# Optimization experiments

Measured on AMD Instinct MI355X. Metric: run time of the kernel, lower is better.

Reference implementation:

```python
import jax, jax.numpy as jnp
import numpy as np

B, S, HID = 1, 4096, 2048
NH, NKV, HD, RD = 16, 4, 128, 64
EPS = 1e-6
SCALE = HD ** -0.5


def _rmsnorm(x, w, eps=EPS):
    x32 = x.astype(jnp.float32)
    var = jnp.mean(x32 * x32, axis=-1, keepdims=True)
    return (w * (x32 * jax.lax.rsqrt(var + eps))).astype(x.dtype)


def _rotate_half(x):
    x1, x2 = jnp.split(x, 2, axis=-1)
    return jnp.concatenate([-x2, x1], axis=-1)


def setup_inputs() -> dict:
    key = jax.random.key(0)
    ks = jax.random.split(key, 6)
    hidden_states = jax.random.normal(ks[0], (B, S, HID), dtype=jnp.float32)
    # real rotary embeddings for rotary_dim=RD
    inv_freq = 1.0 / (10000.0 ** (jnp.arange(0, RD, 2, dtype=jnp.float32) / RD))
    pos = jnp.arange(S, dtype=jnp.float32)
    freqs = pos[:, None] * inv_freq[None, :]          # [S, RD/2]
    emb = jnp.concatenate([freqs, freqs], axis=-1)     # [S, RD]
    cos = jnp.cos(emb)[None]                           # [1, S, RD]
    sin = jnp.sin(emb)[None]
    w = 0.02
    Wq = jax.random.normal(ks[1], (NH * HD, HID), dtype=jnp.float32) * w
    Wk = jax.random.normal(ks[2], (NKV * HD, HID), dtype=jnp.float32) * w
    Wv = jax.random.normal(ks[3], (NKV * HD, HID), dtype=jnp.float32) * w
    Wo = jax.random.normal(ks[4], (HID, NH * HD), dtype=jnp.float32) * w
    q_norm_w = jnp.ones((NH * HD,), dtype=jnp.float32)
    k_norm_w = jnp.ones((NKV * HD,), dtype=jnp.float32)
    return {"hidden_states": hidden_states, "cos": cos, "sin": sin,
            "Wq": Wq, "Wk": Wk, "Wv": Wv, "Wo": Wo,
            "q_norm_w": q_norm_w, "k_norm_w": k_norm_w}


def _attention(hidden_states, cos, sin, Wq, Wk, Wv, Wo, q_norm_w, k_norm_w):
    bsz, q_len, _ = hidden_states.shape
    q = hidden_states @ Wq.T                 # [B,S,NH*HD]
    k = hidden_states @ Wk.T                 # [B,S,NKV*HD]
    v = hidden_states @ Wv.T
    q = _rmsnorm(q, q_norm_w)
    k = _rmsnorm(k, k_norm_w)
    q = q.reshape(bsz, q_len, NH, HD).transpose(0, 2, 1, 3)   # b h s d
    k = k.reshape(bsz, q_len, NKV, HD).transpose(0, 2, 1, 3)
    v = v.reshape(bsz, q_len, NKV, HD).transpose(0, 2, 1, 3)
    # partial RoPE on first RD dims
    c = cos[:, None]  # [B,1,S,RD]
    s = sin[:, None]
    q_rot, q_pass = q[..., :RD], q[..., RD:]
    k_rot, k_pass = k[..., :RD], k[..., RD:]
    q = jnp.concatenate([q_rot * c + _rotate_half(q_rot) * s, q_pass], axis=-1)
    k = jnp.concatenate([k_rot * c + _rotate_half(k_rot) * s, k_pass], axis=-1)
    # GQA: repeat kv heads
    n_rep = NH // NKV
    k = jnp.repeat(k, n_rep, axis=1)
    v = jnp.repeat(v, n_rep, axis=1)
    scores = jnp.einsum('bhqd,bhkd->bhqk', q, k) * SCALE
    causal = jnp.triu(jnp.full((q_len, q_len), -jnp.inf, dtype=scores.dtype), k=1)
    scores = scores + causal
    probs = jax.nn.softmax(scores.astype(jnp.float32), axis=-1).astype(q.dtype)
    out = jnp.einsum('bhqk,bhkd->bhqd', probs, v)
    out = out.transpose(0, 2, 1, 3).reshape(bsz, q_len, NH * HD)
    return out @ Wo.T


def reference(hidden_states, cos, sin, Wq, Wk, Wv, Wo, q_norm_w, k_norm_w):
    return _attention(hidden_states, cos, sin, Wq, Wk, Wv, Wo, q_norm_w, k_norm_w)
```

## Files before the change

kernel.cpp:

```cpp
#include <hip/hip_runtime.h>

typedef unsigned short u16;
typedef unsigned int   u32;
typedef __bf16 bf16x8 __attribute__((ext_vector_type(8)));
typedef float  f32x4  __attribute__((ext_vector_type(4)));

#define S_LEN 4096
#define HIDN  2048
#define NHEAD 16
#define NKVH  4
#define HDIM  128
#define ROTD  64
#define QKVN  3072

__device__ __forceinline__ u16 f2bf(float f) {
  union { float f; u32 u; } v; v.f = f;
  u32 r = v.u + 0x7FFFu + ((v.u >> 16) & 1u);
  return (u16)(r >> 16);
}
__device__ __forceinline__ u16 f2bf_fast(float f) {
  union { __bf16 b; u16 u; } cv; cv.b = (__bf16)f; return cv.u;
}
__device__ __forceinline__ float bf2f(u16 u) {
  union { u32 u; float f; } v; v.u = ((u32)u) << 16; return v.f;
}
__device__ __forceinline__ void gl2lds16(const u16* g, u16* l) {
  __builtin_amdgcn_global_load_lds((const __attribute__((address_space(1))) void*)g,
                                   (__attribute__((address_space(3))) void*)l, 16, 0, 0);
}
__device__ __forceinline__ f32x4 mfma_bf16(bf16x8 a, bf16x8 b, f32x4 c) {
  return __builtin_amdgcn_mfma_f32_16x16x32_bf16(a, b, c, 0, 0, 0);
}
template <int N> __device__ __forceinline__ void vmwait() {
  if constexpr (N == 7)      asm volatile("s_waitcnt vmcnt(7)" ::: "memory");
  else if constexpr (N == 6) asm volatile("s_waitcnt vmcnt(6)" ::: "memory");
  else                       asm volatile("s_waitcnt vmcnt(0)" ::: "memory");
}

__global__ __launch_bounds__(256) void cvt4_f32_bf16(const float* __restrict__ h,
                                                     const float* __restrict__ Wq,
                                                     const float* __restrict__ Wk,
                                                     const float* __restrict__ Wv,
                                                     u16* __restrict__ hbf,
                                                     u16* __restrict__ wqkv) {
  const int b = blockIdx.x;
  const float* src; u16* dst;
  if (b < 4096)      { src = h  + (size_t)b * 2048;           dst = hbf  + (size_t)b * 2048; }
  else if (b < 6144) { src = Wq + (size_t)(b - 4096) * 2048;  dst = wqkv + (size_t)(b - 4096) * 2048; }
  else if (b < 6656) { src = Wk + (size_t)(b - 6144) * 2048;  dst = wqkv + 4194304u + (size_t)(b - 6144) * 2048; }
  else               { src = Wv + (size_t)(b - 6656) * 2048;  dst = wqkv + 5242880u + (size_t)(b - 6656) * 2048; }
  size_t i = (size_t)threadIdx.x * 8;
  float4 a = *(const float4*)(src + i);
  float4 c = *(const float4*)(src + i + 4);
  uint4 r;
  r.x = (u32)f2bf(a.x) | ((u32)f2bf(a.y) << 16);
  r.y = (u32)f2bf(a.z) | ((u32)f2bf(a.w) << 16);
  r.z = (u32)f2bf(c.x) | ((u32)f2bf(c.y) << 16);
  r.w = (u32)f2bf(c.z) | ((u32)f2bf(c.w) << 16);
  *(uint4*)(dst + i) = r;
}

__global__ __launch_bounds__(256) void cvt_f32_bf16(const float* __restrict__ in,
                                                    u16* __restrict__ out) {
  size_t i = ((size_t)blockIdx.x * 256 + threadIdx.x) * 8;
  float4 a = *(const float4*)(in + i);
  float4 b = *(const float4*)(in + i + 4);
  uint4 r;
  r.x = (u32)f2bf(a.x) | ((u32)f2bf(a.y) << 16);
  r.y = (u32)f2bf(a.z) | ((u32)f2bf(a.w) << 16);
  r.z = (u32)f2bf(b.x) | ((u32)f2bf(b.y) << 16);
  r.w = (u32)f2bf(b.z) | ((u32)f2bf(b.w) << 16);
  *(uint4*)(out + i) = r;
}

template <int BN, int NB, bool BF16OUT>
__global__ __launch_bounds__(512, 2) void gemm_big(const u16* __restrict__ A,
                                                   const u16* __restrict__ Bm,
                                                   void* __restrict__ Cp,
                                                   int M, int N, int K) {
  constexpr int WNC = BN / 4;
  constexpr int NF  = WNC / 16;
  constexpr int ASZ = 256 * 128;
  constexpr int BUF = ASZ + BN * 128;
  constexpr int LOADS = 4 + NB;
  __shared__ __align__(1024) char lds[2 * BUF];

  const int tid = threadIdx.x, wave = tid >> 6, lane = tid & 63;
  const int wm = wave >> 2, wn = wave & 3;
  const int row0 = blockIdx.x * 256, col0 = blockIdx.y * BN;
  const int l8 = lane >> 3, l7 = lane & 7;
  const int T = K >> 6;

  const u16* gA[4]; const u16* gB[NB];
  u16* ldsA[4]; u16* ldsB[NB];
  #pragma unroll
  for (int i = 0; i < 4; ++i) {
    gA[i]  = A + (size_t)(row0 + wave * 32 + i * 8 + l8) * K + (l7 ^ l8) * 8;
    ldsA[i] = (u16*)(lds + wave * 4096 + i * 1024);
  }
  #pragma unroll
  for (int i = 0; i < NB; ++i) {
    gB[i]  = Bm + (size_t)(col0 + wave * (BN / 8) + i * 8 + l8) * K + (l7 ^ l8) * 8;
    ldsB[i] = (u16*)(lds + ASZ + wave * (BN * 16) + i * 1024);
  }
  auto stage = [&](int buf, int t) {
    const size_t ko = (size_t)t * 64;
    #pragma unroll
    for (int i = 0; i < 4; ++i)
      gl2lds16(gA[i] + ko, (u16*)((char*)ldsA[i] + buf * BUF));
    #pragma unroll
    for (int i = 0; i < NB; ++i)
      gl2lds16(gB[i] + ko, (u16*)((char*)ldsB[i] + buf * BUF));
  };

  const int colx0 = (((lane >> 4))     ^ l7) * 16;
  const int colx1 = ((4 + (lane >> 4)) ^ l7) * 16;
  const char* aB = lds + (wm * 128 + (lane & 15)) * 128;
  const char* bB = lds + ASZ + (wn * WNC + (lane & 15)) * 128;

  f32x4 acc[8][NF];
  #pragma unroll
  for (int i = 0; i < 8; ++i)
    #pragma unroll
    for (int j = 0; j < NF; ++j) { f32x4 z = {0.f,0.f,0.f,0.f}; acc[i][j] = z; }

  stage(0, 0);
  stage(1, 1);
  vmwait<LOADS>();
  __builtin_amdgcn_s_barrier();

  for (int t = 0; t < T; ++t) {
    const int bo = (t & 1) * BUF;
    #pragma unroll
    for (int kh = 0; kh < 2; ++kh) {
      const int cx = kh ? colx1 : colx0;
      bf16x8 bfr[NF];
      #pragma unroll
      for (int nf = 0; nf < NF; ++nf)
        bfr[nf] = *(const bf16x8*)(bB + bo + nf * 2048 + cx);
      #pragma unroll
      for (int mh = 0; mh < 2; ++mh) {
        bf16x8 af[4];
        #pragma unroll
        for (int mf = 0; mf < 4; ++mf)
          af[mf] = *(const bf16x8*)(aB + bo + mh * 8192 + mf * 2048 + cx);
        __builtin_amdgcn_s_barrier();
        asm volatile("s_waitcnt lgkmcnt(0)" ::: "memory");
        __builtin_amdgcn_s_setprio(1);
        #pragma unroll
        for (int mf = 0; mf < 4; ++mf)
          #pragma unroll
          for (int nf = 0; nf < NF; ++nf)
            acc[mh * 4 + mf][nf] = mfma_bf16(af[mf], bfr[nf], acc[mh * 4 + mf][nf]);
        __builtin_amdgcn_s_setprio(0);
        __builtin_amdgcn_s_barrier();
      }
    }
    if (t + 2 < T) stage(t & 1, t + 2);
    if (t + 1 < T) {
      if (t + 2 < T) vmwait<LOADS>();
      else           vmwait<0>();
      __builtin_amdgcn_s_barrier();
    }
  }

  const int mwv = row0 + wm * 128, nwv = col0 + wn * WNC;
  #pragma unroll
  for (int mf8 = 0; mf8 < 8; ++mf8)
    #pragma unroll
    for (int nf = 0; nf < NF; ++nf)
      #pragma unroll
      for (int r = 0; r < 4; ++r) {
        int m = mwv + (mf8 >> 2) * 64 + (mf8 & 3) * 16 + (lane >> 4) * 4 + r;
        int n = nwv + nf * 16 + (lane & 15);
        float v = acc[mf8][nf][r];
        if (BF16OUT) ((u16*)Cp)[(size_t)m * N + n] = f2bf_fast(v);
        else         ((float*)Cp)[(size_t)m * N + n] = v;
      }
}

__global__ __launch_bounds__(256) void norm_rope(const u16* __restrict__ qkv,
                                                 const float* __restrict__ cosb,
                                                 const float* __restrict__ sinb,
                                                 const float* __restrict__ qw,
                                                 const float* __restrict__ kw,
                                                 u16* __restrict__ Qo,
                                                 u16* __restrict__ Ko) {
  const int s = blockIdx.x, t = threadIdx.x;
  const int wave = t >> 6, lane = t & 63;
  const float SL = 0.08838834764831845f * 1.4426950408889634f;
  __shared__ float rowbuf[HIDN];
  __shared__ float red[4];
  const u16* base = qkv + (size_t)s * QKVN;

  float x[8];
  {
    uint4 v = *(const uint4*)(base + t * 8);
    u32 w4[4] = {v.x, v.y, v.z, v.w};
    #pragma unroll
    for (int j = 0; j < 4; ++j) {
      x[2*j]   = bf2f((u16)(w4[j] & 0xffffu));
      x[2*j+1] = bf2f((u16)(w4[j] >> 16));
    }
  }
  float ss = 0.f;
  #pragma unroll
  for (int j = 0; j < 8; ++j) ss += x[j] * x[j];
  #pragma unroll
  for (int m = 1; m < 64; m <<= 1) ss += __shfl_xor(ss, m);
  if (lane == 0) red[wave] = ss;
  __syncthreads();
  float rs = rsqrtf((red[0]+red[1]+red[2]+red[3]) * (1.0f / HIDN) + 1e-6f);
  #pragma unroll
  for (int j = 0; j < 8; ++j) rowbuf[t*8 + j] = x[j] * rs * qw[t*8 + j];
  __syncthreads();
  {
    int i0 = t * 8, d0 = i0 & (HDIM - 1), hh = i0 >> 7;
    float o[8];
    if (d0 < ROTD) {
      #pragma unroll
      for (int j = 0; j < 8; ++j) {
        int d = d0 + j;
        float rot = (d < 32) ? -rowbuf[i0 + j + 32] : rowbuf[i0 + j - 32];
        o[j] = rowbuf[i0 + j] * cosb[s*ROTD + d] + rot * sinb[s*ROTD + d];
      }
    } else {
      #pragma unroll
      for (int j = 0; j < 8; ++j) o[j] = rowbuf[i0 + j];
    }
    uint4 r;
    r.x = (u32)f2bf(o[0]*SL) | ((u32)f2bf(o[1]*SL) << 16);
    r.y = (u32)f2bf(o[2]*SL) | ((u32)f2bf(o[3]*SL) << 16);
    r.z = (u32)f2bf(o[4]*SL) | ((u32)f2bf(o[5]*SL) << 16);
    r.w = (u32)f2bf(o[6]*SL) | ((u32)f2bf(o[7]*SL) << 16);
    *(uint4*)(Qo + ((size_t)hh * S_LEN + s) * HDIM + d0) = r;
  }

  const u16* kbase = base + HIDN;
  float y0, y1;
  { u32 v = *(const u32*)(kbase + t * 2); y0 = bf2f((u16)(v & 0xffffu)); y1 = bf2f((u16)(v >> 16)); }
  float ss2 = y0*y0 + y1*y1;
  #pragma unroll
  for (int m = 1; m < 64; m <<= 1) ss2 += __shfl_xor(ss2, m);
  __syncthreads();
  if (lane == 0) red[wave] = ss2;
  __syncthreads();
  float rs2 = rsqrtf((red[0]+red[1]+red[2]+red[3]) * (1.0f / 512.0f) + 1e-6f);
  rowbuf[t*2]     = y0 * rs2 * kw[t*2];
  rowbuf[t*2 + 1] = y1 * rs2 * kw[t*2 + 1];
  __syncthreads();
  {
    int i0 = t * 2, d0 = i0 & (HDIM - 1), hh = i0 >> 7;
    float o0, o1;
    if (d0 < ROTD) {
      float r0 = (d0 < 32) ? -rowbuf[i0 + 32] : rowbuf[i0 - 32];
      float r1 = (d0 + 1 < 32) ? -rowbuf[i0 + 1 + 32] : rowbuf[i0 + 1 - 32];
      o0 = rowbuf[i0]     * cosb[s*ROTD + d0]     + r0 * sinb[s*ROTD + d0];
      o1 = rowbuf[i0 + 1] * cosb[s*ROTD + d0 + 1] + r1 * sinb[s*ROTD + d0 + 1];
    } else { o0 = rowbuf[i0]; o1 = rowbuf[i0 + 1]; }
    u32 r = (u32)f2bf(o0) | ((u32)f2bf(o1) << 16);
    *(u32*)(Ko + ((size_t)hh * S_LEN + s) * HDIM + d0) = r;
  }
}

__global__ __launch_bounds__(256) void vtrans(const u16* __restrict__ qkv,
                                              u16* __restrict__ Vt) {
  const int sb = blockIdx.x * 64, db = blockIdx.y * 64, kvh = blockIdx.z;
  __shared__ u16 tile[64][72];
  const int t = threadIdx.x;
  {
    int r = t >> 2, cc = (t & 3) * 16;
    const u16* src = qkv + (size_t)(sb + r) * QKVN + 2560 + kvh * HDIM + db + cc;
    *(uint4*)&tile[r][cc]     = *(const uint4*)(src);
    *(uint4*)&tile[r][cc + 8] = *(const uint4*)(src + 8);
  }
  __syncthreads();
  {
    int d = t >> 2, sc = (t & 3) * 16;
    u16 tmp[16];
    #pragma unroll
    for (int j = 0; j < 16; ++j) tmp[j] = tile[sc + j][d];
    u16* dst = Vt + ((size_t)kvh * HDIM + db + d) * S_LEN + sb + sc;
    *(uint4*)dst       = *(uint4*)&tmp[0];
    *(uint4*)(dst + 8) = *(uint4*)&tmp[8];
  }
}

__global__ __launch_bounds__(256, 2) void attn_fwd(const u16* __restrict__ Q,
                                                   const u16* __restrict__ K,
                                                   const u16* __restrict__ Vt,
                                                   u16* __restrict__ O) {
  const int n    = blockIdx.x;
  const int slot = n & 7, kq = n >> 3;
  const int kvh  = slot >> 1;
  const int h    = kvh * 4 + (slot & 1) * 2 + (kq & 1);
  const int p    = kq >> 1;
  const int tid = threadIdx.x, wave = tid >> 6, lane = tid & 63;
  const int rh   = wave & 1;
  const int kvh2 = wave >> 1;
  __shared__ u16 Ks[2][64][128];
  __shared__ u16 Vs[2][128][64];
  __shared__ u16 Ps[2][32][64];

  const u16* gKb[4]; const u16* gVb[4];
  #pragma unroll
  for (int i = 0; i < 4; ++i) {
    int cc = wave * 4 + i;
    int rk = cc * 4 + (lane >> 4);
    gKb[i] = K + ((size_t)kvh * S_LEN + rk) * HDIM + ((lane & 15) ^ (rk & 7)) * 8;
    int rv = cc * 8 + (lane >> 3);
    gVb[i] = Vt + ((size_t)kvh * HDIM + rv) * S_LEN + ((lane & 7) ^ (rv & 7)) * 8;
  }
  auto stage = [&](int buf, int kvb) {
    #pragma unroll
    for (int i = 0; i < 4; ++i) {
      int cc = wave * 4 + i;
      gl2lds16(gKb[i] + (size_t)kvb * HDIM, &Ks[buf][cc * 4][0]);
      gl2lds16(gVb[i] + kvb,                &Vs[buf][cc * 8][0]);
    }
  };

  int offv[4];
  #pragma unroll
  for (int kk = 0; kk < 4; ++kk)
    offv[kk] = (kk * 64 + (lane >> 4) * 16) ^ ((lane & 7) << 4);
  const char* ksB = (const char*)Ks + kvh2 * 8192 + (lane & 15) * 256;
  const char* vsB = (const char*)Vs + (lane & 15) * 128;
  const char* psB = (const char*)Ps + rh * 4096 + (lane & 15) * 128;
  char*       pwB = (char*)Ps + rh * 4096;
  const int   lx2 = (lane & 15) * 2;
  const int   vko = offv[kvh2];

  stage(0, 0);
  __syncthreads();
  int cur = 0;

  for (int job = 0; job < 2; ++job) {
    const int qb = job ? (63 - p) : p;
    const int ntiles = qb + 1;
    const int qg0 = qb * 64 + rh * 32 + (lane >> 4) * 4;

    bf16x8 qf[2][4];
    #pragma unroll
    for (int qm = 0; qm < 2; ++qm) {
      const u16* qptr = Q + ((size_t)h * S_LEN + qb * 64 + rh * 32 + qm * 16 + (lane & 15)) * HDIM
                        + (lane >> 4) * 8;
      #pragma unroll
      for (int kk = 0; kk < 4; ++kk) qf[qm][kk] = *(const bf16x8*)(qptr + kk * 32);
    }

    float lsum[2][4];
    #pragma unroll
    for (int qm = 0; qm < 2; ++qm)
      #pragma unroll
      for (int r = 0; r < 4; ++r) lsum[qm][r] = 0.f;
    f32x4 o[2][8];
    #pragma unroll
    for (int qm = 0; qm < 2; ++qm)
      #pragma unroll
      for (int i = 0; i < 8; ++i) { f32x4 z = {0.f,0.f,0.f,0.f}; o[qm][i] = z; }

    for (int kt = 0; kt < ntiles; ++kt) {
      if (kt + 1 < ntiles)      stage(cur ^ 1, (kt + 1) * 64);
      else if (job == 0)        stage(cur ^ 1, 0);

      const int bufo = cur << 14;
      const bool diag = (kt == ntiles - 1);

      if (!(diag && kvh2 == 1 && rh == 0)) {
        f32x4 sc[2][2];
        #pragma unroll
        for (int qm = 0; qm < 2; ++qm)
          #pragma unroll
          for (int i = 0; i < 2; ++i) { f32x4 z = {0.f,0.f,0.f,0.f}; sc[qm][i] = z; }
        __builtin_amdgcn_s_setprio(1);
        #pragma unroll
        for (int kk = 0; kk < 4; ++kk)
          #pragma unroll
          for (int nf = 0; nf < 2; ++nf) {
            bf16x8 kf = *(const bf16x8*)(ksB + bufo + nf * 4096 + offv[kk]);
            sc[0][nf] = mfma_bf16(qf[0][kk], kf, sc[0][nf]);
            sc[1][nf] = mfma_bf16(qf[1][kk], kf, sc[1][nf]);
          }
        __builtin_amdgcn_s_setprio(0);

        if (diag) {
          const int kvb = kt * 64;
          #pragma unroll
          for (int qm = 0; qm < 2; ++qm)
            #pragma unroll
            for (int nf = 0; nf < 2; ++nf) {
              int col = kvb + kvh2 * 32 + nf * 16 + (lane & 15);
              #pragma unroll
              for (int r = 0; r < 4; ++r) {
                float e = __builtin_amdgcn_exp2f(sc[qm][nf][r]);
                e = (col <= qg0 + qm * 16 + r) ? e : 0.f;
                sc[qm][nf][r] = e;
                lsum[qm][r] += e;
              }
            }
        } else {
          #pragma unroll
          for (int qm = 0; qm < 2; ++qm)
            #pragma unroll
            for (int nf = 0; nf < 2; ++nf)
              #pragma unroll
              for (int r = 0; r < 4; ++r) {
                float e = __builtin_amdgcn_exp2f(sc[qm][nf][r]);
                sc[qm][nf][r] = e;
                lsum[qm][r] += e;
              }
        }

        #pragma unroll
        for (int qm = 0; qm < 2; ++qm)
          #pragma unroll
          for (int nf = 0; nf < 2; ++nf)
            #pragma unroll
            for (int r = 0; r < 4; ++r) {
              int prow = qm * 16 + (lane >> 4) * 4 + r;
              int bcol = (kvh2 * 64 + nf * 32 + lx2) ^ ((prow & 7) << 4);
              *(u16*)(pwB + prow * 128 + bcol) = f2bf_fast(sc[qm][nf][r]);
            }

        bf16x8 pf0, pf1;
        pf0 = *(const bf16x8*)(psB + vko);
        pf1 = *(const bf16x8*)(psB + 2048 + vko);
        __builtin_amdgcn_s_setprio(1);
        #pragma unroll
        for (int nf2 = 0; nf2 < 8; ++nf2) {
          bf16x8 vf = *(const bf16x8*)(vsB + bufo + nf2 * 2048 + vko);
          o[0][nf2] = mfma_bf16(pf0, vf, o[0][nf2]);
          o[1][nf2] = mfma_bf16(pf1, vf, o[1][nf2]);
        }
        __builtin_amdgcn_s_setprio(0);
      }

      __syncthreads();
      cur ^= 1;
    }

    {
      f32x4* scr = (f32x4*)((rh == 0) ? (char*)Ks + (cur ^ 1) * 16384
                                      : (char*)Vs + (cur ^ 1) * 16384);
      float* lsc = (float*)Ps;
      if (kvh2 == 1) {
        #pragma unroll
        for (int qm = 0; qm < 2; ++qm)
          #pragma unroll
          for (int nf2 = 0; nf2 < 8; ++nf2)
            scr[(qm * 8 + nf2) * 64 + lane] = o[qm][nf2];
        #pragma unroll
        for (int qm = 0; qm < 2; ++qm)
          #pragma unroll
          for (int r = 0; r < 4; ++r)
            lsc[rh * 512 + (qm * 4 + r) * 64 + lane] = lsum[qm][r];
      }
      __syncthreads();
      if (kvh2 == 0) {
        #pragma unroll
        for (int qm = 0; qm < 2; ++qm)
          #pragma unroll
          for (int nf2 = 0; nf2 < 8; ++nf2)
            o[qm][nf2] += scr[(qm * 8 + nf2) * 64 + lane];
        #pragma unroll
        for (int qm = 0; qm < 2; ++qm)
          #pragma unroll
          for (int r = 0; r < 4; ++r)
            lsum[qm][r] += lsc[rh * 512 + (qm * 4 + r) * 64 + lane];

        #pragma unroll
        for (int qm = 0; qm < 2; ++qm)
          #pragma unroll
          for (int r = 0; r < 4; ++r) {
            float lt = lsum[qm][r];
            #pragma unroll
            for (int m = 1; m < 16; m <<= 1) lt += __shfl_xor(lt, m);
            float inv = 1.f / lt;
            int srow = qg0 + qm * 16 + r;
            #pragma unroll
            for (int nf2 = 0; nf2 < 8; ++nf2) {
              int col = h * HDIM + nf2 * 16 + (lane & 15);
              O[(size_t)srow * HIDN + col] = f2bf_fast(o[qm][nf2][r] * inv);
            }
          }
      }
      __syncthreads();
    }
  }
}

extern "C" void kernel_launch(void* const* d_in, const int* in_sizes, int n_in,
                              void* d_out, int out_size, void* d_ws, size_t ws_size,
                              hipStream_t stream) {
  (void)in_sizes; (void)n_in; (void)out_size; (void)ws_size;
  const float* h    = (const float*)d_in[0];
  const float* cosb = (const float*)d_in[1];
  const float* sinb = (const float*)d_in[2];
  const float* Wq   = (const float*)d_in[3];
  const float* Wk   = (const float*)d_in[4];
  const float* Wv   = (const float*)d_in[5];
  const float* Wo   = (const float*)d_in[6];
  const float* qw   = (const float*)d_in[7];
  const float* kw   = (const float*)d_in[8];
  float* out = (float*)d_out;

  char* ws = (char*)d_ws;
  u16* hbf  = (u16*)(ws);
  u16* Kb   = (u16*)(ws + (16u << 20));
  u16* Vtb  = (u16*)(ws + (20u << 20));
  u16* wqkv = (u16*)(ws + (24u << 20));
  u16* Qb   = (u16*)(ws + (24u << 20));
  u16* qkvb = (u16*)(ws + (40u << 20));
  u16* wob  = (u16*)(ws + (40u << 20));

  cvt4_f32_bf16<<<7168, 256, 0, stream>>>(h, Wq, Wk, Wv, hbf, wqkv);

  gemm_big<192, 3, true><<<dim3(16, 16), 512, 0, stream>>>(hbf, wqkv, qkvb,
                                                           4096, 3072, 2048);

  norm_rope<<<4096, 256, 0, stream>>>(qkvb, cosb, sinb, qw, kw, Qb, Kb);
  vtrans<<<dim3(64, 2, 4), 256, 0, stream>>>(qkvb, Vtb);

  cvt_f32_bf16<<<2048, 256, 0, stream>>>(Wo, wob);

  attn_fwd<<<dim3(512), 256, 0, stream>>>(Qb, Kb, Vtb, hbf);

  gemm_big<128, 2, false><<<dim3(16, 16), 512, 0, stream>>>(hbf, wob, out,
                                                            4096, 2048, 2048);
}
```

Before: 240.5 us.

## Load V fragments directly from global into registers; use hardware bf16 conversion

The attention kernel stops staging V tiles through LDS. Each wave now loads its V MFMA fragments straight from the transposed V buffer in global memory at the start of each KV tile, and a dedicated LDS scratch array replaces the reuse of the old V buffer for the final reduction. This cuts LDS traffic and staging work, but adds uncoalesced-ish global loads with latency exposed inside the loop, plus register pressure from 8 bf16x8 fragments. Separately, the manual round-to-nearest-even bf16 conversion is replaced by the compiler's native __bf16 cast in all conversion kernels.

Result: slower. 288.6 us (+20.0%).

```diff
diff --git a/kernel.cpp b/kernel.cpp
--- a/kernel.cpp
+++ b/kernel.cpp
@@ -13,11 +13,6 @@
 #define ROTD  64
 #define QKVN  3072
 
-__device__ __forceinline__ u16 f2bf(float f) {
-  union { float f; u32 u; } v; v.f = f;
-  u32 r = v.u + 0x7FFFu + ((v.u >> 16) & 1u);
-  return (u16)(r >> 16);
-}
 __device__ __forceinline__ u16 f2bf_fast(float f) {
   union { __bf16 b; u16 u; } cv; cv.b = (__bf16)f; return cv.u;
 }
@@ -53,10 +48,10 @@
   float4 a = *(const float4*)(src + i);
   float4 c = *(const float4*)(src + i + 4);
   uint4 r;
-  r.x = (u32)f2bf(a.x) | ((u32)f2bf(a.y) << 16);
-  r.y = (u32)f2bf(a.z) | ((u32)f2bf(a.w) << 16);
-  r.z = (u32)f2bf(c.x) | ((u32)f2bf(c.y) << 16);
-  r.w = (u32)f2bf(c.z) | ((u32)f2bf(c.w) << 16);
+  r.x = (u32)f2bf_fast(a.x) | ((u32)f2bf_fast(a.y) << 16);
+  r.y = (u32)f2bf_fast(a.z) | ((u32)f2bf_fast(a.w) << 16);
+  r.z = (u32)f2bf_fast(c.x) | ((u32)f2bf_fast(c.y) << 16);
+  r.w = (u32)f2bf_fast(c.z) | ((u32)f2bf_fast(c.w) << 16);
   *(uint4*)(dst + i) = r;
 }
 
@@ -66,10 +61,10 @@
   float4 a = *(const float4*)(in + i);
   float4 b = *(const float4*)(in + i + 4);
   uint4 r;
-  r.x = (u32)f2bf(a.x) | ((u32)f2bf(a.y) << 16);
-  r.y = (u32)f2bf(a.z) | ((u32)f2bf(a.w) << 16);
-  r.z = (u32)f2bf(b.x) | ((u32)f2bf(b.y) << 16);
-  r.w = (u32)f2bf(b.z) | ((u32)f2bf(b.w) << 16);
+  r.x = (u32)f2bf_fast(a.x) | ((u32)f2bf_fast(a.y) << 16);
+  r.y = (u32)f2bf_fast(a.z) | ((u32)f2bf_fast(a.w) << 16);
+  r.z = (u32)f2bf_fast(b.x) | ((u32)f2bf_fast(b.y) << 16);
+  r.w = (u32)f2bf_fast(b.z) | ((u32)f2bf_fast(b.w) << 16);
   *(uint4*)(out + i) = r;
 }
 
@@ -229,10 +224,10 @@
       for (int j = 0; j < 8; ++j) o[j] = rowbuf[i0 + j];
     }
     uint4 r;
-    r.x = (u32)f2bf(o[0]*SL) | ((u32)f2bf(o[1]*SL) << 16);
-    r.y = (u32)f2bf(o[2]*SL) | ((u32)f2bf(o[3]*SL) << 16);
-    r.z = (u32)f2bf(o[4]*SL) | ((u32)f2bf(o[5]*SL) << 16);
-    r.w = (u32)f2bf(o[6]*SL) | ((u32)f2bf(o[7]*SL) << 16);
+    r.x = (u32)f2bf_fast(o[0]*SL) | ((u32)f2bf_fast(o[1]*SL) << 16);
+    r.y = (u32)f2bf_fast(o[2]*SL) | ((u32)f2bf_fast(o[3]*SL) << 16);
+    r.z = (u32)f2bf_fast(o[4]*SL) | ((u32)f2bf_fast(o[5]*SL) << 16);
+    r.w = (u32)f2bf_fast(o[6]*SL) | ((u32)f2bf_fast(o[7]*SL) << 16);
     *(uint4*)(Qo + ((size_t)hh * S_LEN + s) * HDIM + d0) = r;
   }
 
@@ -258,7 +253,7 @@
       o0 = rowbuf[i0]     * cosb[s*ROTD + d0]     + r0 * sinb[s*ROTD + d0];
       o1 = rowbuf[i0 + 1] * cosb[s*ROTD + d0 + 1] + r1 * sinb[s*ROTD + d0 + 1];
     } else { o0 = rowbuf[i0]; o1 = rowbuf[i0 + 1]; }
-    u32 r = (u32)f2bf(o0) | ((u32)f2bf(o1) << 16);
+    u32 r = (u32)f2bf_fast(o0) | ((u32)f2bf_fast(o1) << 16);
     *(u32*)(Ko + ((size_t)hh * S_LEN + s) * HDIM + d0) = r;
   }
 }
@@ -299,33 +294,32 @@
   const int rh   = wave & 1;
   const int kvh2 = wave >> 1;
   __shared__ u16 Ks[2][64][128];
-  __shared__ u16 Vs[2][128][64];
+  __shared__ f32x4 scrb[2][1024];
   __shared__ u16 Ps[2][32][64];
 
-  const u16* gKb[4]; const u16* gVb[4];
+  const u16* gKb[4];
   #pragma unroll
   for (int i = 0; i < 4; ++i) {
     int cc = wave * 4 + i;
     int rk = cc * 4 + (lane >> 4);
     gKb[i] = K + ((size_t)kvh * S_LEN + rk) * HDIM + ((lane & 15) ^ (rk & 7)) * 8;
-    int rv = cc * 8 + (lane >> 3);
-    gVb[i] = Vt + ((size_t)kvh * HDIM + rv) * S_LEN + ((lane & 7) ^ (rv & 7)) * 8;
   }
   auto stage = [&](int buf, int kvb) {
     #pragma unroll
     for (int i = 0; i < 4; ++i) {
       int cc = wave * 4 + i;
       gl2lds16(gKb[i] + (size_t)kvb * HDIM, &Ks[buf][cc * 4][0]);
-      gl2lds16(gVb[i] + kvb,                &Vs[buf][cc * 8][0]);
     }
   };
+
+  const u16* gVt = Vt + ((size_t)kvh * HDIM + (lane & 15)) * S_LEN
+                   + kvh2 * 32 + (lane >> 4) * 8;
 
   int offv[4];
   #pragma unroll
   for (int kk = 0; kk < 4; ++kk)
     offv[kk] = (kk * 64 + (lane >> 4) * 16) ^ ((lane & 7) << 4);
   const char* ksB = (const char*)Ks + kvh2 * 8192 + (lane & 15) * 256;
-  const char* vsB = (const char*)Vs + (lane & 15) * 128;
   const char* psB = (const char*)Ps + rh * 4096 + (lane & 15) * 128;
   char*       pwB = (char*)Ps + rh * 4096;
   const int   lx2 = (lane & 15) * 2;
@@ -361,13 +355,24 @@
       for (int i = 0; i < 8; ++i) { f32x4 z = {0.f,0.f,0.f,0.f}; o[qm][i] = z; }
 
     for (int kt = 0; kt < ntiles; ++kt) {
+      const int kvb = kt * 64;
+      const bool diag = (kt == ntiles - 1);
+      const bool act  = !(diag && kvh2 == 1 && rh == 0);
+
+      bf16x8 vf[8];
+      if (act) {
+        const u16* gv = gVt + kvb;
+        #pragma unroll
+        for (int nf2 = 0; nf2 < 8; ++nf2)
+          vf[nf2] = *(const bf16x8*)(gv + (size_t)nf2 * 16 * S_LEN);
+      }
+
       if (kt + 1 < ntiles)      stage(cur ^ 1, (kt + 1) * 64);
       else if (job == 0)        stage(cur ^ 1, 0);
 
       const int bufo = cur << 14;
-      const bool diag = (kt == ntiles - 1);
-
-      if (!(diag && kvh2 == 1 && rh == 0)) {
+
+      if (act) {
         f32x4 sc[2][2];
         #pragma unroll
         for (int qm = 0; qm < 2; ++qm)
@@ -385,7 +390,6 @@
         __builtin_amdgcn_s_setprio(0);
 
         if (diag) {
-          const int kvb = kt * 64;
           #pragma unroll
           for (int qm = 0; qm < 2; ++qm)
             #pragma unroll
@@ -423,15 +427,13 @@
               *(u16*)(pwB + prow * 128 + bcol) = f2bf_fast(sc[qm][nf][r]);
             }
 
-        bf16x8 pf0, pf1;
-        pf0 = *(const bf16x8*)(psB + vko);
-        pf1 = *(const bf16x8*)(psB + 2048 + vko);
+        bf16x8 pf0 = *(const bf16x8*)(psB + vko);
+        bf16x8 pf1 = *(const bf16x8*)(psB + 2048 + vko);
         __builtin_amdgcn_s_setprio(1);
         #pragma unroll
         for (int nf2 = 0; nf2 < 8; ++nf2) {
-          bf16x8 vf = *(const bf16x8*)(vsB + bufo + nf2 * 2048 + vko);
-          o[0][nf2] = mfma_bf16(pf0, vf, o[0][nf2]);
-          o[1][nf2] = mfma_bf16(pf1, vf, o[1][nf2]);
+          o[0][nf2] = mfma_bf16(pf0, vf[nf2], o[0][nf2]);
+          o[1][nf2] = mfma_bf16(pf1, vf[nf2], o[1][nf2]);
         }
         __builtin_amdgcn_s_setprio(0);
       }
@@ -441,8 +443,7 @@
     }
 
     {
-      f32x4* scr = (f32x4*)((rh == 0) ? (char*)Ks + (cur ^ 1) * 16384
-                                      : (char*)Vs + (cur ^ 1) * 16384);
+      f32x4* scr = &scrb[rh][0];
       float* lsc = (float*)Ps;
       if (kvh2 == 1) {
         #pragma unroll
```
